# Performance work log

Hardware: AMD Instinct MI355X
Metric: run time of the kernel (lower is better)

## Reference

```python
import jax, jax.numpy as jnp
from jax import lax
import numpy as np

B, K, T, C, E = 64, 32, 1280, 16, 64
CONV_CH, POOL = 32, 10


def setup_inputs() -> dict:
    key = jax.random.key(0)
    ks = jax.random.split(key, 10)
    inp = {
        "x": jax.random.normal(ks[0], (B, T, C), dtype=jnp.float32),
        # learnable prototypes (torch inits to zeros; random here for a meaningful baseline)
        "prototypes": jax.random.normal(ks[1], (K, T, C), dtype=jnp.float32) * 0.1,
        "conv_w": jax.random.normal(ks[2], (CONV_CH, C, 5), dtype=jnp.float32) * (1.0 / np.sqrt(C * 5)),
        "conv_b": jax.random.normal(ks[3], (CONV_CH,), dtype=jnp.float32) * 0.01,
        "lin_w": jax.random.normal(ks[4], (E, CONV_CH * POOL), dtype=jnp.float32) * (1.0 / np.sqrt(CONV_CH * POOL)),
        "lin_b": jax.random.normal(ks[5], (E,), dtype=jnp.float32) * 0.01,
        # stacked per-class Linear(E,1) predictors: rows = classes
        "warp_W": jax.random.normal(ks[6], (K, E), dtype=jnp.float32) * (1.0 / np.sqrt(E)),
        "warp_b": jax.random.normal(ks[7], (K,), dtype=jnp.float32) * 0.01,
        "off_W": jax.random.normal(ks[8], (K, E), dtype=jnp.float32) * (1.0 / np.sqrt(E)),
        "off_b": jax.random.normal(ks[9], (K,), dtype=jnp.float32) * 0.01,
    }
    return inp


def _forward(x, prototypes, conv_w, conv_b, lin_w, lin_b, warp_W, warp_b, off_W, off_b):
    b, t, c = x.shape
    k = prototypes.shape[0]
    # encoder: Conv1d -> ReLU -> AdaptiveAvgPool1d(10) -> Flatten -> Linear -> ReLU
    h = lax.conv_general_dilated(
        jnp.transpose(x, (0, 2, 1)), conv_w, window_strides=(1,),
        padding=[(2, 2)], dimension_numbers=("NCH", "OIH", "NCH"))
    h = jax.nn.relu(h + conv_b[None, :, None])  # [B, 32, T]
    h = h.reshape(b, CONV_CH, POOL, t // POOL).mean(-1)  # adaptive avg pool (T % 10 == 0)
    embed = jax.nn.relu(h.reshape(b, CONV_CH * POOL) @ lin_w.T + lin_b)  # [B, E]
    # per-class scalar warp / offset predictions
    warp = embed @ warp_W.T + warp_b  # [B, K]
    off = embed @ off_W.T + off_b     # [B, K]
    aligned = prototypes[None] + off[:, :, None, None]  # [B, K, T, C]
    # batched 1D linear-interpolation warp (replaces nested python loops)
    base = jnp.arange(t, dtype=x.dtype)
    idx = jnp.clip(base[None, None, :] - warp[:, :, None], 0.0, t - 1)  # [B, K, T]
    idx0f = jnp.floor(idx)
    i0 = idx0f.astype(jnp.int32)
    i1 = jnp.clip(i0 + 1, 0, t - 1)
    frac = (idx - idx0f)[..., None]  # [B, K, T, 1]
    g0 = jnp.take_along_axis(aligned, i0[..., None], axis=2)  # [B, K, T, C]
    g1 = jnp.take_along_axis(aligned, i1[..., None], axis=2)
    warped = g0 * (1.0 - frac) + g1 * frac
    return warped, warp[..., None], off[..., None]


def reference(x, prototypes, conv_w, conv_b, lin_w, lin_b, warp_W, warp_b, off_W, off_b):
    return _forward(x, prototypes, conv_w, conv_b, lin_w, lin_b, warp_W, warp_b, off_W, off_b)
```

## Files before the change

### kernel.cpp

```cpp
#include <hip/hip_runtime.h>
#include <hip/hip_bf16.h>

constexpr int B_ = 64, K_ = 32, T_ = 1280, C_ = 16, E_ = 64;
constexpr int CC_ = 32, POOL_ = 10, TB_ = 128;
constexpr long long OUT_WARPED = (long long)B_ * K_ * T_ * C_;

__global__ __launch_bounds__(256) void conv_pool_k(
    const float* __restrict__ x,
    const float* __restrict__ conv_w,
    const float* __restrict__ conv_b,
    float* __restrict__ pooled)
{
    const int blk = blockIdx.x;
    const int b = blk / POOL_;
    const int p = blk % POOL_;
    const int tid = threadIdx.x;

    __shared__ float xs[132 * 20];
    __shared__ float wt[32 * 84];
    __shared__ float part[256];

    for (int f = tid; f < CC_ * C_ * 5; f += 256) {
        int oc = f / 80, r = f % 80, ic = r / 5, kt = r % 5;
        wt[oc * 84 + kt * 16 + ic] = conv_w[f];
    }
    const float4* x4 = (const float4*)(x + (size_t)b * T_ * C_);
    for (int f = tid; f < 132 * 4; f += 256) {
        int row = f >> 2, c4 = f & 3;
        int t = p * TB_ - 2 + row;
        float4 v = make_float4(0.f, 0.f, 0.f, 0.f);
        if (t >= 0 && t < T_) v = x4[t * 4 + c4];
        *(float4*)(&xs[row * 20 + c4 * 4]) = v;
    }
    __syncthreads();

    const int oc = tid >> 3;
    const int tsub = tid & 7;

    float4 w[5][4];
#pragma unroll
    for (int kt = 0; kt < 5; ++kt)
#pragma unroll
        for (int c4 = 0; c4 < 4; ++c4)
            w[kt][c4] = *(const float4*)(&wt[oc * 84 + kt * 16 + c4 * 4]);
    const float bias = conv_b[oc];

    const int base = tsub * 16;
    float4 win[5][4];
#pragma unroll
    for (int r = 0; r < 4; ++r)
#pragma unroll
        for (int c4 = 0; c4 < 4; ++c4)
            win[r][c4] = *(const float4*)(&xs[(base + r) * 20 + c4 * 4]);

    float local = 0.f;
#pragma unroll
    for (int jj = 0; jj < 16; ++jj) {
        const int ld = (jj + 4) % 5;
#pragma unroll
        for (int c4 = 0; c4 < 4; ++c4)
            win[ld][c4] = *(const float4*)(&xs[(base + jj + 4) * 20 + c4 * 4]);
        float acc = bias;
#pragma unroll
        for (int kt = 0; kt < 5; ++kt) {
            const float4* xv = win[(jj + kt) % 5];
#pragma unroll
            for (int c4 = 0; c4 < 4; ++c4) {
                acc += xv[c4].x * w[kt][c4].x;
                acc += xv[c4].y * w[kt][c4].y;
                acc += xv[c4].z * w[kt][c4].z;
                acc += xv[c4].w * w[kt][c4].w;
            }
        }
        local += fmaxf(acc, 0.f);
    }

    part[tid] = local;
    __syncthreads();
    if (tid < CC_) {
        float s = 0.f;
#pragma unroll
        for (int i = 0; i < 8; ++i) s += part[tid * 8 + i];
        pooled[b * (CC_ * POOL_) + tid * POOL_ + p] = s * (1.f / 128.f);
    }
}

__global__ __launch_bounds__(64) void heads_k(
    const float* __restrict__ pooled,
    const float* __restrict__ lin_w,
    const float* __restrict__ lin_b,
    const float* __restrict__ warp_W,
    const float* __restrict__ warp_b,
    const float* __restrict__ off_W,
    const float* __restrict__ off_b,
    float* __restrict__ warp_s,
    float* __restrict__ off_s,
    float* __restrict__ out_tail)
{
    const int b = blockIdx.x;
    const int tid = threadIdx.x;
    __shared__ float4 ps4[80];
    __shared__ float emb[64];

    const float4* pin = (const float4*)(pooled + (size_t)b * 320);
    for (int i = tid; i < 80; i += 64) ps4[i] = pin[i];
    __syncthreads();

    float acc = lin_b[tid];
    const float4* lw4 = (const float4*)(lin_w + (size_t)tid * 320);
#pragma unroll 4
    for (int i = 0; i < 80; ++i) {
        float4 a = ps4[i], w = lw4[i];
        acc += a.x * w.x + a.y * w.y + a.z * w.z + a.w * w.w;
    }
    emb[tid] = fmaxf(acc, 0.f);
    __syncthreads();

    const int k = tid & 31;
    const float* W = (tid < 32) ? warp_W : off_W;
    const float* bb = (tid < 32) ? warp_b : off_b;
    float a2 = bb[k];
#pragma unroll 8
    for (int e = 0; e < E_; ++e) a2 += emb[e] * W[k * E_ + e];

    if (tid < 32) {
        warp_s[b * K_ + k] = a2;
        out_tail[b * K_ + k] = a2;
    } else {
        off_s[b * K_ + k] = a2;
        out_tail[B_ * K_ + b * K_ + k] = a2;
    }
}

__global__ __launch_bounds__(256) void warp_interp_k(
    const float* __restrict__ proto,
    const float* __restrict__ warp_s,
    const float* __restrict__ off_s,
    float* __restrict__ out)
{
    const int n = blockIdx.x * 256 + threadIdx.x;
    const int q = n & 3;
    const int row = n >> 2;
    const int t = row % T_;
    const int bk = row / T_;
    const int k = bk & (K_ - 1);

    const float wv = warp_s[bk];
    const float ov = off_s[bk];

    float idx = fminf(fmaxf((float)t - wv, 0.f), (float)(T_ - 1));
    const float f0 = floorf(idx);
    const int i0 = (int)f0;
    const int i1 = min(i0 + 1, T_ - 1);
    const float fr = idx - f0;
    const float omf = 1.f - fr;

    const float4* p4 = (const float4*)proto;
    const float4 g0 = p4[(k * T_ + i0) * 4 + q];
    const float4 g1 = p4[(k * T_ + i1) * 4 + q];

    float4 r;
    r.x = (g0.x + ov) * omf + (g1.x + ov) * fr;
    r.y = (g0.y + ov) * omf + (g1.y + ov) * fr;
    r.z = (g0.z + ov) * omf + (g1.z + ov) * fr;
    r.w = (g0.w + ov) * omf + (g1.w + ov) * fr;

    ((float4*)out)[n] = r;
}

extern "C" void kernel_launch(void* const* d_in, const int* in_sizes, int n_in,
                              void* d_out, int out_size, void* d_ws, size_t ws_size,
                              hipStream_t stream) {
    const float* x       = (const float*)d_in[0];
    const float* proto   = (const float*)d_in[1];
    const float* conv_w  = (const float*)d_in[2];
    const float* conv_b  = (const float*)d_in[3];
    const float* lin_w   = (const float*)d_in[4];
    const float* lin_b   = (const float*)d_in[5];
    const float* warp_W  = (const float*)d_in[6];
    const float* warp_b  = (const float*)d_in[7];
    const float* off_W   = (const float*)d_in[8];
    const float* off_b   = (const float*)d_in[9];

    float* out = (float*)d_out;
    float* ws = (float*)d_ws;
    float* pooled = ws;
    float* warp_s = ws + 20480;
    float* off_s  = ws + 20480 + 2048;

    conv_pool_k<<<dim3(B_ * POOL_), dim3(256), 0, stream>>>(x, conv_w, conv_b, pooled);
    heads_k<<<dim3(B_), dim3(64), 0, stream>>>(pooled, lin_w, lin_b, warp_W, warp_b,
                                               off_W, off_b, warp_s, off_s,
                                               out + OUT_WARPED);
    warp_interp_k<<<dim3((B_ * K_ * T_ * 4) / 256), dim3(256), 0, stream>>>(
        proto, warp_s, off_s, out);
}
```

Baseline: 213.1 us.

## Use one block per (b,k) row in warp interp with nontemporal stores, remap conv threads

The interpolation kernel now launches one block per batch-class pair. Each block loops over all time steps, so the warp and offset scalars are loaded once per block instead of once per thread. The output is written with nontemporal stores so the large streaming write does not pollute the cache. The conv kernel's thread-to-channel mapping is swapped so that adjacent lanes handle different output channels, which changes the LDS access pattern for the input window. Fewer, larger blocks may reduce occupancy and latency hiding.

```diff
diff --git a/kernel.cpp b/kernel.cpp
--- a/kernel.cpp
+++ b/kernel.cpp
@@ -4,6 +4,8 @@
 constexpr int B_ = 64, K_ = 32, T_ = 1280, C_ = 16, E_ = 64;
 constexpr int CC_ = 32, POOL_ = 10, TB_ = 128;
 constexpr long long OUT_WARPED = (long long)B_ * K_ * T_ * C_;
+
+typedef float floatx4 __attribute__((ext_vector_type(4)));
 
 __global__ __launch_bounds__(256) void conv_pool_k(
     const float* __restrict__ x,
@@ -34,8 +36,8 @@
     }
     __syncthreads();
 
-    const int oc = tid >> 3;
-    const int tsub = tid & 7;
+    const int oc = tid & 31;
+    const int tsub = tid >> 5;
 
     float4 w[5][4];
 #pragma unroll
@@ -80,7 +82,7 @@
     if (tid < CC_) {
         float s = 0.f;
 #pragma unroll
-        for (int i = 0; i < 8; ++i) s += part[tid * 8 + i];
+        for (int i = 0; i < 8; ++i) s += part[i * 32 + tid];
         pooled[b * (CC_ * POOL_) + tid * POOL_ + p] = s * (1.f / 128.f);
     }
 }
@@ -138,34 +140,35 @@
     const float* __restrict__ off_s,
     float* __restrict__ out)
 {
-    const int n = blockIdx.x * 256 + threadIdx.x;
-    const int q = n & 3;
-    const int row = n >> 2;
-    const int t = row % T_;
-    const int bk = row / T_;
+    const int bk = blockIdx.x;
     const int k = bk & (K_ - 1);
+    const int tid = threadIdx.x;
 
     const float wv = warp_s[bk];
     const float ov = off_s[bk];
 
-    float idx = fminf(fmaxf((float)t - wv, 0.f), (float)(T_ - 1));
-    const float f0 = floorf(idx);
-    const int i0 = (int)f0;
-    const int i1 = min(i0 + 1, T_ - 1);
-    const float fr = idx - f0;
-    const float omf = 1.f - fr;
-
-    const float4* p4 = (const float4*)proto;
-    const float4 g0 = p4[(k * T_ + i0) * 4 + q];
-    const float4 g1 = p4[(k * T_ + i1) * 4 + q];
-
-    float4 r;
-    r.x = (g0.x + ov) * omf + (g1.x + ov) * fr;
-    r.y = (g0.y + ov) * omf + (g1.y + ov) * fr;
-    r.z = (g0.z + ov) * omf + (g1.z + ov) * fr;
-    r.w = (g0.w + ov) * omf + (g1.w + ov) * fr;
-
-    ((float4*)out)[n] = r;
+    const floatx4* pk = (const floatx4*)proto + (size_t)k * T_ * 4;
+    floatx4* ob = (floatx4*)out + (size_t)bk * T_ * 4;
+
+#pragma unroll 4
+    for (int m = 0; m < 20; ++m) {
+        const int fi = m * 256 + tid;
+        const int t = fi >> 2;
+        const int q = fi & 3;
+
+        float idx = fminf(fmaxf((float)t - wv, 0.f), (float)(T_ - 1));
+        const float f0 = floorf(idx);
+        const int i0 = (int)f0;
+        const int i1 = min(i0 + 1, T_ - 1);
+        const float fr = idx - f0;
+        const float omf = 1.f - fr;
+
+        const floatx4 g0 = pk[i0 * 4 + q];
+        const floatx4 g1 = pk[i1 * 4 + q];
+
+        floatx4 r = (g0 + ov) * omf + (g1 + ov) * fr;
+        __builtin_nontemporal_store(r, &ob[fi]);
+    }
 }
 
 extern "C" void kernel_launch(void* const* d_in, const int* in_sizes, int n_in,
@@ -192,6 +195,6 @@
     heads_k<<<dim3(B_), dim3(64), 0, stream>>>(pooled, lin_w, lin_b, warp_W, warp_b,
                                                off_W, off_b, warp_s, off_s,
                                                out + OUT_WARPED);
-    warp_interp_k<<<dim3((B_ * K_ * T_ * 4) / 256), dim3(256), 0, stream>>>(
+    warp_interp_k<<<dim3(B_ * K_), dim3(256), 0, stream>>>(
         proto, warp_s, off_s, out);
 }
```

Result: slower. 219.3 us (+2.9%).
